# Kernel optimization log

Measured on AMD Instinct MI355X. Metric: run time of the kernel, lower is better.

The kernel has to match this reference:

```python
import jax, jax.numpy as jnp
import numpy as np

WINDOW = 1024


def _dft_weights(window):
    # w[k, n] = exp(-2*pi*i*k*n/window); torch module stores real/imag parts as conv weights
    n = np.arange(window)
    ang = -2.0 * np.pi * (n[:, None] * n[None, :]) / window  # [K, N] in float64 like numpy
    return np.cos(ang).astype(np.float32), np.sin(ang).astype(np.float32)


def setup_inputs() -> dict:
    key = jax.random.key(0)
    k1, k2, k3, k4 = jax.random.split(key, 4)
    w_real, w_imag = _dft_weights(WINDOW)
    bound = 1.0 / np.sqrt(WINDOW)  # torch Conv1d default bias init: U(-1/sqrt(fan_in), 1/sqrt(fan_in))
    return {
        "x_r": jax.random.normal(k1, (8, 4096, WINDOW), dtype=jnp.float32),
        "x_i": jax.random.normal(k2, (8, 4096, WINDOW), dtype=jnp.float32),
        "w_real": jnp.asarray(w_real),
        "w_imag": jnp.asarray(w_imag),
        "b_real": jax.random.uniform(k3, (WINDOW,), minval=-bound, maxval=bound, dtype=jnp.float32),
        "b_imag": jax.random.uniform(k4, (WINDOW,), minval=-bound, maxval=bound, dtype=jnp.float32),
    }


def reference(x_r, x_i, w_real, w_imag, b_real, b_imag):
    # Conv1d with full-window kernel == matmul over the last axis.
    # conv_real(x) = x @ w_real.T + b_real ; conv_imag(x) = x @ w_imag.T + b_imag
    xr_wr = jnp.einsum('bfn,kn->bfk', x_r, w_real)
    xr_wi = jnp.einsum('bfn,kn->bfk', x_r, w_imag)
    xi_wr = jnp.einsum('bfn,kn->bfk', x_i, w_real)
    xi_wi = jnp.einsum('bfn,kn->bfk', x_i, w_imag)
    real = (xr_wr + b_real) - (xi_wi + b_imag)
    imag = (xr_wi + b_imag) + (xi_wr + b_real)
    return (real, imag)
```

## Files before the change

### kernel.cpp

```cpp
#include <hip/hip_runtime.h>
#include <stdint.h>

#define NFFT  1024
#define MROWS 32768
#define GRID  2048

__device__ __forceinline__ int P(int i) { return i + (i >> 4); }

__device__ __forceinline__ void dft4(float& ar, float& ai, float& br_, float& bi_,
                                     float& cr, float& ci, float& dr, float& di) {
  const float t0r = ar + cr,  t0i = ai + ci;
  const float t1r = ar - cr,  t1i = ai - ci;
  const float t2r = br_ + dr, t2i = bi_ + di;
  const float t3r = bi_ - di, t3i = dr - br_;
  ar  = t0r + t2r; ai  = t0i + t2i;
  br_ = t1r + t3r; bi_ = t1i + t3i;
  cr  = t0r - t2r; ci  = t0i - t2i;
  dr  = t1r - t3r; di  = t1i - t3i;
}

__device__ __forceinline__ void cmul(float& xr, float& xi, float c, float s) {
  const float r = xr * c - xi * s;
  xi = xr * s + xi * c;
  xr = r;
}

__global__ void __launch_bounds__(256, 4)
fft1024(const float* __restrict__ xr, const float* __restrict__ xi,
        const float* __restrict__ wr, const float* __restrict__ wi,
        const float* __restrict__ br, const float* __restrict__ bi,
        float* __restrict__ out) {
  __shared__ __align__(16) float twr[256], twi[256];
  __shared__ __align__(16) float lds[4 * 2176];

  const int tid = threadIdx.x;
  const int w   = tid >> 6;
  const int t   = tid & 63;
  float* buf = lds + w * 2176;
  const int b  = t & 15;
  const int a  = t >> 4;
  const int t4 = t << 2;

  twr[tid] = wr[NFFT + tid];
  twi[tid] = wi[NFFT + tid];
  __syncthreads();

  const float u1r = wr[NFFT +  64], u1i = wi[NFFT +  64];
  const float u2r = wr[NFFT + 128], u2i = wi[NFFT + 128];
  const float u3r = wr[NFFT + 192], u3i = wi[NFFT + 192];
  const float u4r = wr[NFFT + 256], u4i = wi[NFFT + 256];
  const float u6r = wr[NFFT + 384], u6i = wi[NFFT + 384];
  const float u9r = wr[NFFT + 576], u9i = wi[NFFT + 576];

#pragma unroll 1
  for (int row = blockIdx.x * 4 + w; row < MROWS; row += GRID * 4) {
    const float* pr = xr + (size_t)row * NFFT;
    const float* px = xi + (size_t)row * NFFT;

    float vr[16], vi[16];
#pragma unroll
    for (int q = 0; q < 4; ++q)
#pragma unroll
      for (int r = 0; r < 4; ++r) {
        vr[q + 4 * r] = pr[t + 64 * (q + 4 * r)];
        vi[q + 4 * r] = px[t + 64 * (q + 4 * r)];
      }

#pragma unroll
    for (int q = 0; q < 4; ++q)
      dft4(vr[q], vi[q], vr[q + 4], vi[q + 4], vr[q + 8], vi[q + 8], vr[q + 12], vi[q + 12]);

    cmul(vr[5],  vi[5],  u1r, u1i);  cmul(vr[6],  vi[6],  u2r, u2i);
    cmul(vr[7],  vi[7],  u3r, u3i);
    cmul(vr[9],  vi[9],  u2r, u2i);  cmul(vr[10], vi[10], u4r, u4i);
    cmul(vr[11], vi[11], u6r, u6i);
    cmul(vr[13], vi[13], u3r, u3i);  cmul(vr[14], vi[14], u6r, u6i);
    cmul(vr[15], vi[15], u9r, u9i);
#pragma unroll
    for (int m = 0; m < 4; ++m)
      dft4(vr[4 * m], vi[4 * m], vr[1 + 4 * m], vi[1 + 4 * m],
           vr[2 + 4 * m], vi[2 + 4 * m], vr[3 + 4 * m], vi[3 + 4 * m]);

#pragma unroll
    for (int u = 0; u < 16; ++u) {
      const int m = u & 3, k1 = u >> 2;
      *(float2*)&buf[2 * P(16 * t + u)] = make_float2(vr[k1 + 4 * m], vi[k1 + 4 * m]);
    }
    asm volatile("" ::: "memory");

#pragma unroll
    for (int q = 0; q < 4; ++q)
#pragma unroll
      for (int r = 0; r < 4; ++r) {
        const float2 f = *(const float2*)&buf[2 * P(t + 64 * q + 256 * r)];
        vr[q + 4 * r] = f.x; vi[q + 4 * r] = f.y;
      }
    asm volatile("" ::: "memory");
    {
      const float c1 = twr[16 * b], s1 = twi[16 * b];
      const float c2 = c1 * c1 - s1 * s1, s2 = 2.f * c1 * s1;
      const float c3 = c2 * c1 - s2 * s1, s3 = c2 * s1 + s2 * c1;
#pragma unroll
      for (int q = 0; q < 4; ++q) {
        cmul(vr[q + 4],  vi[q + 4],  c1, s1);
        cmul(vr[q + 8],  vi[q + 8],  c2, s2);
        cmul(vr[q + 12], vi[q + 12], c3, s3);
        dft4(vr[q], vi[q], vr[q + 4], vi[q + 4], vr[q + 8], vi[q + 8], vr[q + 12], vi[q + 12]);
      }
    }

#pragma unroll
    for (int k2 = 0; k2 < 4; ++k2) {
      const float c1 = twr[4 * (b + 16 * k2)], s1 = twi[4 * (b + 16 * k2)];
      const float c2 = c1 * c1 - s1 * s1, s2 = 2.f * c1 * s1;
      const float c3 = c2 * c1 - s2 * s1, s3 = c2 * s1 + s2 * c1;
      cmul(vr[1 + 4 * k2], vi[1 + 4 * k2], c1, s1);
      cmul(vr[2 + 4 * k2], vi[2 + 4 * k2], c2, s2);
      cmul(vr[3 + 4 * k2], vi[3 + 4 * k2], c3, s3);
      dft4(vr[4 * k2], vi[4 * k2], vr[1 + 4 * k2], vi[1 + 4 * k2],
           vr[2 + 4 * k2], vi[2 + 4 * k2], vr[3 + 4 * k2], vi[3 + 4 * k2]);
    }

#pragma unroll
    for (int k2 = 0; k2 < 4; ++k2)
#pragma unroll
      for (int k3 = 0; k3 < 4; ++k3)
        *(float2*)&buf[2 * P(256 * a + b + 16 * k2 + 64 * k3)] =
            make_float2(vr[k3 + 4 * k2], vi[k3 + 4 * k2]);
    asm volatile("" ::: "memory");

#pragma unroll
    for (int m = 0; m < 4; ++m)
#pragma unroll
      for (int r = 0; r < 4; ++r) {
        const float2 f = *(const float2*)&buf[2 * P(t4 + m + 256 * r)];
        vr[m + 4 * r] = f.x; vi[m + 4 * r] = f.y;
      }
    asm volatile("" ::: "memory");
    {
      const float4 C = *(const float4*)&twr[t4];
      const float4 S = *(const float4*)&twi[t4];
      const float cc[4] = {C.x, C.y, C.z, C.w};
      const float ss[4] = {S.x, S.y, S.z, S.w};
#pragma unroll
      for (int m = 0; m < 4; ++m) {
        const float c1 = cc[m], s1 = ss[m];
        const float c2 = c1 * c1 - s1 * s1, s2 = 2.f * c1 * s1;
        const float c3 = c2 * c1 - s2 * s1, s3 = c2 * s1 + s2 * c1;
        cmul(vr[m + 4],  vi[m + 4],  c1, s1);
        cmul(vr[m + 8],  vi[m + 8],  c2, s2);
        cmul(vr[m + 12], vi[m + 12], c3, s3);
        dft4(vr[m], vi[m], vr[m + 4], vi[m + 4], vr[m + 8], vi[m + 8], vr[m + 12], vi[m + 12]);
      }
    }

    float* o_r = out + (size_t)row * NFFT;
    float* o_i = out + (size_t)MROWS * NFFT + (size_t)row * NFFT;
#pragma unroll
    for (int k = 0; k < 4; ++k) {
      const float4 fb = *(const float4*)(br + t4 + 256 * k);
      const float4 gb = *(const float4*)(bi + t4 + 256 * k);
      float4 R, I;
      R.x = vr[0 + 4 * k] + fb.x - gb.x; I.x = vi[0 + 4 * k] + fb.x + gb.x;
      R.y = vr[1 + 4 * k] + fb.y - gb.y; I.y = vi[1 + 4 * k] + fb.y + gb.y;
      R.z = vr[2 + 4 * k] + fb.z - gb.z; I.z = vi[2 + 4 * k] + fb.z + gb.z;
      R.w = vr[3 + 4 * k] + fb.w - gb.w; I.w = vi[3 + 4 * k] + fb.w + gb.w;
      *(float4*)(o_r + t4 + 256 * k) = R;
      *(float4*)(o_i + t4 + 256 * k) = I;
    }
  }
}

extern "C" void kernel_launch(void* const* d_in, const int* in_sizes, int n_in,
                              void* d_out, int out_size, void* d_ws, size_t ws_size,
                              hipStream_t stream) {
  const float* xr = (const float*)d_in[0];
  const float* xi = (const float*)d_in[1];
  const float* wr = (const float*)d_in[2];
  const float* wi = (const float*)d_in[3];
  const float* br = (const float*)d_in[4];
  const float* bi = (const float*)d_in[5];
  float* out = (float*)d_out;
  (void)in_sizes; (void)n_in; (void)out_size; (void)d_ws; (void)ws_size;

  fft1024<<<GRID, 256, 0, stream>>>(xr, xi, wr, wi, br, bi, out);
}
```

Baseline: 492.2 us.

## Prefetch next row into registers, hoist bias, widen LDS accesses with new padding

Software-pipelines the row loop by loading the next row's 32 input values into registers while the current row's FFT stages run. The per-lane bias sums are computed once and kept in registers. Twiddles are interleaved into a float2 table, and LDS padding changes to two slots per 16 so stores and loads can use float4. The aim is to hide global load latency in a memory-bound kernel and cut LDS instruction count. The cost is many more live registers, which could lower occupancy under launch_bounds(256,4) or cause spills.

```diff
diff --git a/kernel.cpp b/kernel.cpp
--- a/kernel.cpp
+++ b/kernel.cpp
@@ -1,11 +1,12 @@
 #include <hip/hip_runtime.h>
 #include <stdint.h>
 
-#define NFFT  1024
-#define MROWS 32768
-#define GRID  2048
-
-__device__ __forceinline__ int P(int i) { return i + (i >> 4); }
+#define NFFT    1024
+#define MROWS   32768
+#define GRID    2048
+#define RSTRIDE (GRID * 4)
+
+__device__ __forceinline__ int P2(int i) { return i + 2 * (i >> 4); }
 
 __device__ __forceinline__ void dft4(float& ar, float& ai, float& br_, float& bi_,
                                      float& cr, float& ci, float& dr, float& di) {
@@ -30,19 +31,18 @@
         const float* __restrict__ wr, const float* __restrict__ wi,
         const float* __restrict__ br, const float* __restrict__ bi,
         float* __restrict__ out) {
-  __shared__ __align__(16) float twr[256], twi[256];
-  __shared__ __align__(16) float lds[4 * 2176];
+  __shared__ __align__(16) float2 tw2[256];
+  __shared__ __align__(16) float lds[4 * 2304];
 
   const int tid = threadIdx.x;
   const int w   = tid >> 6;
   const int t   = tid & 63;
-  float* buf = lds + w * 2176;
+  float* buf = lds + w * 2304;
   const int b  = t & 15;
   const int a  = t >> 4;
   const int t4 = t << 2;
 
-  twr[tid] = wr[NFFT + tid];
-  twi[tid] = wi[NFFT + tid];
+  tw2[tid] = make_float2(wr[NFFT + tid], wi[NFFT + tid]);
   __syncthreads();
 
   const float u1r = wr[NFFT +  64], u1i = wi[NFFT +  64];
@@ -52,23 +52,50 @@
   const float u6r = wr[NFFT + 384], u6i = wi[NFFT + 384];
   const float u9r = wr[NFFT + 576], u9i = wi[NFFT + 576];
 
-#pragma unroll 1
-  for (int row = blockIdx.x * 4 + w; row < MROWS; row += GRID * 4) {
+  float badd_r[4][4], badd_i[4][4];
+#pragma unroll
+  for (int k = 0; k < 4; ++k) {
+    const float4 fb = *(const float4*)(br + t4 + 256 * k);
+    const float4 gb = *(const float4*)(bi + t4 + 256 * k);
+    badd_r[k][0] = fb.x - gb.x; badd_i[k][0] = fb.x + gb.x;
+    badd_r[k][1] = fb.y - gb.y; badd_i[k][1] = fb.y + gb.y;
+    badd_r[k][2] = fb.z - gb.z; badd_i[k][2] = fb.z + gb.z;
+    badd_r[k][3] = fb.w - gb.w; badd_i[k][3] = fb.w + gb.w;
+  }
+
+  int row = blockIdx.x * 4 + w;
+  float pvr[16], pvi[16];
+  {
     const float* pr = xr + (size_t)row * NFFT;
     const float* px = xi + (size_t)row * NFFT;
+#pragma unroll
+    for (int e = 0; e < 16; ++e) { pvr[e] = pr[t + 64 * e]; pvi[e] = px[t + 64 * e]; }
+  }
+
+#pragma unroll 1
+  for (; row < MROWS; ) {
+    const int nxt = row + RSTRIDE;
 
     float vr[16], vi[16];
 #pragma unroll
-    for (int q = 0; q < 4; ++q)
-#pragma unroll
-      for (int r = 0; r < 4; ++r) {
-        vr[q + 4 * r] = pr[t + 64 * (q + 4 * r)];
-        vi[q + 4 * r] = px[t + 64 * (q + 4 * r)];
-      }
-
-#pragma unroll
-    for (int q = 0; q < 4; ++q)
-      dft4(vr[q], vi[q], vr[q + 4], vi[q + 4], vr[q + 8], vi[q + 8], vr[q + 12], vi[q + 12]);
+    for (int q = 0; q < 4; ++q) {
+      float e0r = pvr[q],      e0i = pvi[q];
+      float e1r = pvr[q + 4],  e1i = pvi[q + 4];
+      float e2r = pvr[q + 8],  e2i = pvi[q + 8];
+      float e3r = pvr[q + 12], e3i = pvi[q + 12];
+      dft4(e0r, e0i, e1r, e1i, e2r, e2i, e3r, e3i);
+      vr[q]      = e0r; vi[q]      = e0i;
+      vr[q + 4]  = e1r; vi[q + 4]  = e1i;
+      vr[q + 8]  = e2r; vi[q + 8]  = e2i;
+      vr[q + 12] = e3r; vi[q + 12] = e3i;
+    }
+
+    if (nxt < MROWS) {
+      const float* pr = xr + (size_t)nxt * NFFT;
+      const float* px = xi + (size_t)nxt * NFFT;
+#pragma unroll
+      for (int e = 0; e < 16; ++e) { pvr[e] = pr[t + 64 * e]; pvi[e] = px[t + 64 * e]; }
+    }
 
     cmul(vr[5],  vi[5],  u1r, u1i);  cmul(vr[6],  vi[6],  u2r, u2i);
     cmul(vr[7],  vi[7],  u3r, u3i);
@@ -82,9 +109,13 @@
            vr[2 + 4 * m], vi[2 + 4 * m], vr[3 + 4 * m], vi[3 + 4 * m]);
 
 #pragma unroll
-    for (int u = 0; u < 16; ++u) {
-      const int m = u & 3, k1 = u >> 2;
-      *(float2*)&buf[2 * P(16 * t + u)] = make_float2(vr[k1 + 4 * m], vi[k1 + 4 * m]);
+    for (int jj = 0; jj < 8; ++jj) {
+      const int u0 = 2 * jj, u1_ = 2 * jj + 1;
+      const int e0 = (u0 >> 2) + 4 * (u0 & 3);
+      const int e1 = (u1_ >> 2) + 4 * (u1_ & 3);
+      float4 f;
+      f.x = vr[e0]; f.y = vi[e0]; f.z = vr[e1]; f.w = vi[e1];
+      *(float4*)&buf[2 * (18 * t + u0)] = f;
     }
     asm volatile("" ::: "memory");
 
@@ -92,12 +123,13 @@
     for (int q = 0; q < 4; ++q)
 #pragma unroll
       for (int r = 0; r < 4; ++r) {
-        const float2 f = *(const float2*)&buf[2 * P(t + 64 * q + 256 * r)];
+        const float2 f = *(const float2*)&buf[2 * P2(t + 64 * q + 256 * r)];
         vr[q + 4 * r] = f.x; vi[q + 4 * r] = f.y;
       }
     asm volatile("" ::: "memory");
     {
-      const float c1 = twr[16 * b], s1 = twi[16 * b];
+      const float2 T = tw2[16 * b];
+      const float c1 = T.x, s1 = T.y;
       const float c2 = c1 * c1 - s1 * s1, s2 = 2.f * c1 * s1;
       const float c3 = c2 * c1 - s2 * s1, s3 = c2 * s1 + s2 * c1;
 #pragma unroll
@@ -111,7 +143,8 @@
 
 #pragma unroll
     for (int k2 = 0; k2 < 4; ++k2) {
-      const float c1 = twr[4 * (b + 16 * k2)], s1 = twi[4 * (b + 16 * k2)];
+      const float2 T = tw2[4 * (b + 16 * k2)];
+      const float c1 = T.x, s1 = T.y;
       const float c2 = c1 * c1 - s1 * s1, s2 = 2.f * c1 * s1;
       const float c3 = c2 * c1 - s2 * s1, s3 = c2 * s1 + s2 * c1;
       cmul(vr[1 + 4 * k2], vi[1 + 4 * k2], c1, s1);
@@ -125,23 +158,24 @@
     for (int k2 = 0; k2 < 4; ++k2)
 #pragma unroll
       for (int k3 = 0; k3 < 4; ++k3)
-        *(float2*)&buf[2 * P(256 * a + b + 16 * k2 + 64 * k3)] =
+        *(float2*)&buf[2 * P2(256 * a + b + 16 * k2 + 64 * k3)] =
             make_float2(vr[k3 + 4 * k2], vi[k3 + 4 * k2]);
     asm volatile("" ::: "memory");
 
 #pragma unroll
-    for (int m = 0; m < 4; ++m)
-#pragma unroll
-      for (int r = 0; r < 4; ++r) {
-        const float2 f = *(const float2*)&buf[2 * P(t4 + m + 256 * r)];
-        vr[m + 4 * r] = f.x; vi[m + 4 * r] = f.y;
+    for (int r = 0; r < 4; ++r)
+#pragma unroll
+      for (int jj = 0; jj < 2; ++jj) {
+        const float4 f = *(const float4*)&buf[2 * P2(t4 + 2 * jj + 256 * r)];
+        vr[2 * jj + 0 + 4 * r] = f.x; vi[2 * jj + 0 + 4 * r] = f.y;
+        vr[2 * jj + 1 + 4 * r] = f.z; vi[2 * jj + 1 + 4 * r] = f.w;
       }
     asm volatile("" ::: "memory");
     {
-      const float4 C = *(const float4*)&twr[t4];
-      const float4 S = *(const float4*)&twi[t4];
-      const float cc[4] = {C.x, C.y, C.z, C.w};
-      const float ss[4] = {S.x, S.y, S.z, S.w};
+      const float4 T01 = *(const float4*)&tw2[t4];
+      const float4 T23 = *(const float4*)&tw2[t4 + 2];
+      const float cc[4] = {T01.x, T01.z, T23.x, T23.z};
+      const float ss[4] = {T01.y, T01.w, T23.y, T23.w};
 #pragma unroll
       for (int m = 0; m < 4; ++m) {
         const float c1 = cc[m], s1 = ss[m];
@@ -158,16 +192,16 @@
     float* o_i = out + (size_t)MROWS * NFFT + (size_t)row * NFFT;
 #pragma unroll
     for (int k = 0; k < 4; ++k) {
-      const float4 fb = *(const float4*)(br + t4 + 256 * k);
-      const float4 gb = *(const float4*)(bi + t4 + 256 * k);
       float4 R, I;
-      R.x = vr[0 + 4 * k] + fb.x - gb.x; I.x = vi[0 + 4 * k] + fb.x + gb.x;
-      R.y = vr[1 + 4 * k] + fb.y - gb.y; I.y = vi[1 + 4 * k] + fb.y + gb.y;
-      R.z = vr[2 + 4 * k] + fb.z - gb.z; I.z = vi[2 + 4 * k] + fb.z + gb.z;
-      R.w = vr[3 + 4 * k] + fb.w - gb.w; I.w = vi[3 + 4 * k] + fb.w + gb.w;
+      R.x = vr[0 + 4 * k] + badd_r[k][0]; I.x = vi[0 + 4 * k] + badd_i[k][0];
+      R.y = vr[1 + 4 * k] + badd_r[k][1]; I.y = vi[1 + 4 * k] + badd_i[k][1];
+      R.z = vr[2 + 4 * k] + badd_r[k][2]; I.z = vi[2 + 4 * k] + badd_i[k][2];
+      R.w = vr[3 + 4 * k] + badd_r[k][3]; I.w = vi[3 + 4 * k] + badd_i[k][3];
       *(float4*)(o_r + t4 + 256 * k) = R;
       *(float4*)(o_i + t4 + 256 * k) = I;
     }
+
+    row = nxt;
   }
 }
 
```

New measurement: 528.4 us. 7.4% more time.
